# Performance work log

Measured on AMD Instinct MI355X. Metric: run time of the kernel, lower is better.

Reference implementation:

```python
import jax, jax.numpy as jnp
import numpy as np

H, KV, HD = 32, 4, 64
REP = H // KV
MAX_POS = 2048


def setup_inputs() -> dict:
    key = jax.random.key(0)
    ks = jax.random.split(key, 6)
    B, S, D = 2, 1024, 2048
    x = jax.random.normal(ks[0], (B, S, D), dtype=jnp.float32)
    wq = jax.random.normal(ks[1], (D, H * HD), dtype=jnp.float32) * 0.02
    wk = jax.random.normal(ks[2], (D, KV * HD), dtype=jnp.float32) * 0.02
    wv = jax.random.normal(ks[3], (D, KV * HD), dtype=jnp.float32) * 0.02
    wo = jax.random.normal(ks[4], (H * HD, D), dtype=jnp.float32) * 0.02
    # RoPE tables: [max_pos, head_dim//2]
    inv_freq = 1.0 / (10000.0 ** (np.arange(0, HD, 2, dtype=np.float32) / HD))
    angles = np.arange(MAX_POS, dtype=np.float32)[:, None] * inv_freq[None, :]
    cos = jnp.asarray(np.cos(angles), dtype=jnp.float32)
    sin = jnp.asarray(np.sin(angles), dtype=jnp.float32)
    # causal additive mask [S, S]
    row = jnp.arange(S)[:, None]
    col = jnp.arange(S)[None, :]
    mask = jnp.where(col <= row, 0.0, -1e9).astype(jnp.float32)
    return {"x": x, "wq": wq, "wk": wk, "wv": wv, "wo": wo,
            "cos": cos, "sin": sin, "mask": mask, "pos": 0}


def _rotate(t, c, s):
    # t: [B,S,Hx,HD]; c,s: [1,S,1,HD//2]
    half = t.shape[-1] // 2
    t1, t2 = t[..., :half], t[..., half:]
    return jnp.concatenate([t1 * c - t2 * s, t2 * c + t1 * s], axis=-1)


def reference(x, wq, wk, wv, wo, cos, sin, mask, pos):
    B, S, D = x.shape
    q = (x @ wq).reshape(B, S, H, HD)
    k = (x @ wk).reshape(B, S, KV, HD)
    v = (x @ wv).reshape(B, S, KV, HD)
    c = cos[pos:pos + S][None, :, None, :]
    s = sin[pos:pos + S][None, :, None, :]
    q = _rotate(q, c, s)
    k = _rotate(k, c, s)
    # prefill: cache[:, 0:S] == fresh k,v, kv_len == S
    # native GQA broadcast: group q heads by kv head instead of repeating k/v
    qg = q.reshape(B, S, KV, REP, HD)
    scores = jnp.einsum('bqkrd,bskd->bkrqs', qg, k) / jnp.sqrt(jnp.float32(HD))
    scores = scores + mask  # mask broadcasts over [B,KV,REP,S,S]
    attn = jax.nn.softmax(scores, axis=-1)
    out = jnp.einsum('bkrqs,bskd->bqkrd', attn, v).reshape(B, S, H * HD)
    return out @ wo
```

## Files before the change

### kernel.cpp

```cpp
#include <hip/hip_runtime.h>

#define B_ 2
#define S_ 1024
#define D_ 2048
#define H_ 32
#define KV_ 4
#define HD_ 64
#define NQKV 2560
#define KVB 64

typedef __attribute__((ext_vector_type(8))) short bf16x8;
typedef __attribute__((ext_vector_type(4))) float f32x4;
typedef __attribute__((ext_vector_type(16))) float f32x16;

__device__ __forceinline__ unsigned short f2bf(float f) {
  unsigned int u = __float_as_uint(f);
  u = (u + 0x7fffu + ((u >> 16) & 1u)) >> 16;
  return (unsigned short)u;
}

#define GLOAD_LDS(gp, lp) \
  __builtin_amdgcn_global_load_lds((const __attribute__((address_space(1))) void*)(gp), \
                                   (__attribute__((address_space(3))) void*)(lp), 16, 0, 0)

__global__ __launch_bounds__(256) void k_convert(const float* __restrict__ src,
                                                 unsigned short* __restrict__ dst, int n4) {
  int i = blockIdx.x * 256 + threadIdx.x;
  if (i >= n4) return;
  float4 v = ((const float4*)src)[i];
  ushort4 o;
  o.x = f2bf(v.x); o.y = f2bf(v.y); o.z = f2bf(v.z); o.w = f2bf(v.w);
  ((ushort4*)dst)[i] = o;
}

__global__ __launch_bounds__(256) void k_transpose4(const float* __restrict__ wq,
                                                    const float* __restrict__ wk,
                                                    const float* __restrict__ wv,
                                                    const float* __restrict__ wo,
                                                    unsigned short* __restrict__ wft,
                                                    unsigned short* __restrict__ wot) {
  __shared__ float tile[32][33];
  const int z = blockIdx.z;
  const float* src;
  unsigned short* dst;
  int N, roff;
  if (z == 0)      { src = wq; dst = wft; N = 2048; roff = 0; }
  else if (z == 1) { src = wk; dst = wft; N = 256;  roff = 2048; }
  else if (z == 2) { src = wv; dst = wft; N = 256;  roff = 2304; }
  else             { src = wo; dst = wot; N = 2048; roff = 0; }
  int n0 = blockIdx.x * 32, k0 = blockIdx.y * 32;
  if (n0 >= N) return;
  int tx = threadIdx.x & 31, ty = threadIdx.x >> 5;
  #pragma unroll
  for (int i = 0; i < 4; ++i)
    tile[ty + 8 * i][tx] = src[(size_t)(k0 + ty + 8 * i) * N + (n0 + tx)];
  __syncthreads();
  #pragma unroll
  for (int i = 0; i < 4; ++i)
    dst[(size_t)(roff + n0 + ty + 8 * i) * D_ + (k0 + tx)] = f2bf(tile[tx][ty + 8 * i]);
}

template <int BM, int BN, int MODE>
__global__ __launch_bounds__(256) void k_gemm(const unsigned short* __restrict__ A,
                                              const unsigned short* __restrict__ Bt,
                                              float* __restrict__ C,
                                              const float* __restrict__ cosT,
                                              const float* __restrict__ sinT,
                                              const int* __restrict__ posp,
                                              unsigned short* __restrict__ q_r,
                                              unsigned short* __restrict__ k_r,
                                              unsigned short* __restrict__ v_t,
                                              int M, int N, int K) {
  constexpr int MR = BM / 32;
  constexpr int NR = BN / 32;
  __shared__ alignas(16) unsigned short As[BM * 64];
  __shared__ alignas(16) unsigned short Bs[BN * 64];
  const int tid = threadIdx.x;
  const int wid = tid >> 6, lane = tid & 63;
  const int lo = lane & 15, hi = lane >> 4;
  const int m0 = blockIdx.y * BM, n0 = blockIdx.x * BN;
  const int wr = wid >> 1, wc = wid & 1;
  f32x4 acc[MR][NR] = {};

  const int nkt = K >> 6;
  for (int kt = 0; kt < nkt; ++kt) {
    __syncthreads();
    #pragma unroll
    for (int u = tid; u < BM * 8; u += 256) {
      int row = u >> 3, ch = u & 7, chs = ch ^ (row & 7);
      GLOAD_LDS(A + (size_t)(m0 + row) * K + kt * 64 + chs * 8, As + u * 8);
    }
    #pragma unroll
    for (int u = tid; u < BN * 8; u += 256) {
      int row = u >> 3, ch = u & 7, chs = ch ^ (row & 7);
      GLOAD_LDS(Bt + (size_t)(n0 + row) * K + kt * 64 + chs * 8, Bs + u * 8);
    }
    __syncthreads();
    #pragma unroll
    for (int ks = 0; ks < 2; ++ks) {
      const int chs = (ks * 4 + hi) ^ (lo & 7);
      bf16x8 a[MR], b[NR];
      #pragma unroll
      for (int m = 0; m < MR; ++m) {
        int row = wr * (BM / 2) + m * 16 + lo;
        a[m] = *(const bf16x8*)(As + row * 64 + chs * 8);
      }
      #pragma unroll
      for (int n = 0; n < NR; ++n) {
        int row = wc * (BN / 2) + n * 16 + lo;
        b[n] = *(const bf16x8*)(Bs + row * 64 + chs * 8);
      }
      #pragma unroll
      for (int m = 0; m < MR; ++m)
        #pragma unroll
        for (int n = 0; n < NR; ++n)
          acc[m][n] = __builtin_amdgcn_mfma_f32_16x16x32_bf16(a[m], b[n], acc[m][n], 0, 0, 0);
    }
  }

  if (MODE == 0) {
    const int cr = hi * 4;
    #pragma unroll
    for (int m = 0; m < MR; ++m)
      #pragma unroll
      for (int n = 0; n < NR; ++n) {
        int col = n0 + wc * (BN / 2) + n * 16 + lo;
        int rowb = m0 + wr * (BM / 2) + m * 16 + cr;
        #pragma unroll
        for (int r = 0; r < 4; ++r)
          C[(size_t)(rowb + r) * N + col] = acc[m][n][r];
      }
  } else {
    const int col0 = n0 + wc * (BN / 2);
    const int pos = posp[0];
    if (col0 < 2048) {
      const int h = col0 >> 6;
      #pragma unroll
      for (int m = 0; m < MR; ++m)
        #pragma unroll
        for (int r = 0; r < 4; ++r) {
          int row = m0 + wr * (BM / 2) + m * 16 + hi * 4 + r;
          int s = row & (S_ - 1), b = row >> 10;
          unsigned short* base = q_r + ((size_t)(b * H_ + h) * S_ + s) * HD_;
          #pragma unroll
          for (int np = 0; np < 2; ++np) {
            int i = np * 16 + lo;
            float t1 = acc[m][np][r], t2 = acc[m][np + 2][r];
            float c = cosT[(size_t)(pos + s) * 32 + i];
            float sn = sinT[(size_t)(pos + s) * 32 + i];
            base[i] = f2bf((t1 * c - t2 * sn) * 0.125f);
            base[i + 32] = f2bf((t2 * c + t1 * sn) * 0.125f);
          }
        }
    } else if (col0 < 2304) {
      const int g = (col0 - 2048) >> 6;
      #pragma unroll
      for (int m = 0; m < MR; ++m)
        #pragma unroll
        for (int r = 0; r < 4; ++r) {
          int row = m0 + wr * (BM / 2) + m * 16 + hi * 4 + r;
          int s = row & (S_ - 1), b = row >> 10;
          unsigned short* base = k_r + ((size_t)(b * KV_ + g) * S_ + s) * HD_;
          #pragma unroll
          for (int np = 0; np < 2; ++np) {
            int i = np * 16 + lo;
            float t1 = acc[m][np][r], t2 = acc[m][np + 2][r];
            float c = cosT[(size_t)(pos + s) * 32 + i];
            float sn = sinT[(size_t)(pos + s) * 32 + i];
            base[i] = f2bf(t1 * c - t2 * sn);
            base[i + 32] = f2bf(t2 * c + t1 * sn);
          }
        }
    } else {
      const int g = (col0 - 2304) >> 6;
      #pragma unroll
      for (int m = 0; m < MR; ++m) {
        int row0 = m0 + wr * (BM / 2) + m * 16 + hi * 4;
        int s0 = row0 & (S_ - 1), b = row0 >> 10;
        #pragma unroll
        for (int n = 0; n < NR; ++n) {
          int d = n * 16 + lo;
          ushort4 o;
          o.x = f2bf(acc[m][n][0]);
          o.y = f2bf(acc[m][n][1]);
          o.z = f2bf(acc[m][n][2]);
          o.w = f2bf(acc[m][n][3]);
          *(ushort4*)(v_t + ((size_t)(b * KV_ + g) * HD_ + d) * S_ + s0) = o;
        }
      }
    }
  }
}

__global__ __launch_bounds__(256) void k_attn(const unsigned short* __restrict__ qr,
                                              const unsigned short* __restrict__ kr,
                                              const unsigned short* __restrict__ vt,
                                              unsigned short* __restrict__ ao) {
  __shared__ alignas(16) unsigned short k_lds[2][KVB * HD_];
  __shared__ alignas(16) unsigned short v_lds[2][HD_ * KVB];
  const int tid = threadIdx.x;
  const int wid = tid >> 6, lane = tid & 63;
  const int l31 = lane & 31, hi5 = lane >> 5;

  const int fid = blockIdx.x + 8 * blockIdx.y + 256 * blockIdx.z;
  const int half = fid >> 8, u0 = fid & 255;
  const int i4 = u0 >> 6, hb = u0 & 63;
  const int qt = half ? 7 - i4 : i4;
  const int h = hb >> 1, b = hb & 1, g = h >> 3;

  const int q_abs = qt * 128 + wid * 32 + l31;
  const int nch = 2 * qt + 2;

  const unsigned short* qrow = qr + ((size_t)(b * H_ + h) * S_ + q_abs) * HD_;
  bf16x8 qf[4];
  #pragma unroll
  for (int ks = 0; ks < 4; ++ks)
    qf[ks] = *(const bf16x8*)(qrow + ks * 16 + hi5 * 8);

  const unsigned short* kbase = kr + (size_t)(b * KV_ + g) * S_ * HD_;
  const unsigned short* vbase = vt + (size_t)(b * KV_ + g) * HD_ * S_;

  f32x16 oacc[2] = {};
  float mrun = -1e30f, ls = 0.f;
  int buf = 0;

  auto stage = [&](int c, int bi) {
    const int j0 = c * KVB;
    #pragma unroll
    for (int ii = 0; ii < 2; ++ii) {
      int uu = ii * 256 + tid;
      int r = uu >> 3, ch = uu & 7, chs = ch ^ (r & 7);
      GLOAD_LDS(kbase + (size_t)(j0 + r) * HD_ + chs * 8, k_lds[bi] + uu * 8);
    }
    #pragma unroll
    for (int ii = 0; ii < 2; ++ii) {
      int uu = ii * 256 + tid;
      int d = uu >> 3, ch = uu & 7, chs = ch ^ (d & 7);
      GLOAD_LDS(vbase + (size_t)d * S_ + j0 + chs * 8, v_lds[bi] + uu * 8);
    }
  };

  stage(0, 0);
  __syncthreads();

  for (int c = 0; c < nch; ++c) {
    if (c + 1 < nch) stage(c + 1, buf ^ 1);
    const unsigned short* kl = k_lds[buf];
    const unsigned short* vl = v_lds[buf];
    const int j0 = c * KVB;

    f32x16 st[2] = {};
    __builtin_amdgcn_s_setprio(1);
    #pragma unroll
    for (int ks = 0; ks < 4; ++ks) {
      const int chs = ((ks * 2 + hi5) ^ (l31 & 7)) * 8;
      #pragma unroll
      for (int jt = 0; jt < 2; ++jt) {
        bf16x8 kf = *(const bf16x8*)(kl + (jt * 32 + l31) * HD_ + chs);
        st[jt] = __builtin_amdgcn_mfma_f32_32x32x16_bf16(kf, qf[ks], st[jt], 0, 0, 0);
      }
    }
    __builtin_amdgcn_s_setprio(0);

    float pmax = -1e30f;
    if (c >= nch - 2) {
      #pragma unroll
      for (int jt = 0; jt < 2; ++jt)
        #pragma unroll
        for (int r = 0; r < 16; ++r) {
          int j_abs = j0 + jt * 32 + (r & 3) + 8 * (r >> 2) + 4 * hi5;
          if (j_abs > q_abs) st[jt][r] = -1e30f;
          pmax = fmaxf(pmax, st[jt][r]);
        }
    } else {
      #pragma unroll
      for (int jt = 0; jt < 2; ++jt)
        #pragma unroll
        for (int r = 0; r < 16; ++r) pmax = fmaxf(pmax, st[jt][r]);
    }
    pmax = fmaxf(pmax, __shfl_xor(pmax, 32, 64));
    float mn = fmaxf(mrun, pmax);
    float scale = __expf(mrun - mn);
    float lsl = 0.f;
    #pragma unroll
    for (int jt = 0; jt < 2; ++jt)
      #pragma unroll
      for (int r = 0; r < 16; ++r) {
        float e = __expf(st[jt][r] - mn);
        st[jt][r] = e;
        lsl += e;
      }
    ls = ls * scale + lsl;
    mrun = mn;
    #pragma unroll
    for (int dt = 0; dt < 2; ++dt)
      #pragma unroll
      for (int r = 0; r < 16; ++r) oacc[dt][r] *= scale;

    unsigned int pk[2][4][2];
    #pragma unroll
    for (int jt = 0; jt < 2; ++jt)
      #pragma unroll
      for (int qd = 0; qd < 4; ++qd) {
        pk[jt][qd][0] = (unsigned int)f2bf(st[jt][qd * 4 + 0]) |
                        ((unsigned int)f2bf(st[jt][qd * 4 + 1]) << 16);
        pk[jt][qd][1] = (unsigned int)f2bf(st[jt][qd * 4 + 2]) |
                        ((unsigned int)f2bf(st[jt][qd * 4 + 3]) << 16);
      }

    bf16x8 pf[4];
    #pragma unroll
    for (int jt = 0; jt < 2; ++jt) {
      unsigned int ex0a = hi5 ? pk[jt][0][0] : pk[jt][1][0];
      unsigned int ex0b = hi5 ? pk[jt][0][1] : pk[jt][1][1];
      unsigned int ex1a = hi5 ? pk[jt][2][0] : pk[jt][3][0];
      unsigned int ex1b = hi5 ? pk[jt][2][1] : pk[jt][3][1];
      unsigned int rA0 = (unsigned int)__shfl_xor((int)ex0a, 32, 64);
      unsigned int rA1 = (unsigned int)__shfl_xor((int)ex0b, 32, 64);
      unsigned int rB0 = (unsigned int)__shfl_xor((int)ex1a, 32, 64);
      unsigned int rB1 = (unsigned int)__shfl_xor((int)ex1b, 32, 64);
      union { unsigned int w[4]; bf16x8 v; } fe, fo;
      if (hi5) {
        fe.w[0] = rA0; fe.w[1] = rA1; fe.w[2] = pk[jt][1][0]; fe.w[3] = pk[jt][1][1];
        fo.w[0] = rB0; fo.w[1] = rB1; fo.w[2] = pk[jt][3][0]; fo.w[3] = pk[jt][3][1];
      } else {
        fe.w[0] = pk[jt][0][0]; fe.w[1] = pk[jt][0][1]; fe.w[2] = rA0; fe.w[3] = rA1;
        fo.w[0] = pk[jt][2][0]; fo.w[1] = pk[jt][2][1]; fo.w[2] = rB0; fo.w[3] = rB1;
      }
      pf[jt * 2 + 0] = fe.v;
      pf[jt * 2 + 1] = fo.v;
    }

    __builtin_amdgcn_s_setprio(1);
    #pragma unroll
    for (int ks = 0; ks < 4; ++ks) {
      const int chs = ((ks * 2 + hi5) ^ (l31 & 7)) * 8;
      #pragma unroll
      for (int dt = 0; dt < 2; ++dt) {
        bf16x8 vf = *(const bf16x8*)(vl + (dt * 32 + l31) * KVB + chs);
        oacc[dt] = __builtin_amdgcn_mfma_f32_32x32x16_bf16(vf, pf[ks], oacc[dt], 0, 0, 0);
      }
    }
    __builtin_amdgcn_s_setprio(0);

    __syncthreads();
    buf ^= 1;
  }

  float tot = ls + __shfl_xor(ls, 32, 64);
  float inv = 1.f / tot;
  unsigned short* orow = ao + (size_t)(b * S_ + q_abs) * (H_ * HD_) + h * HD_;
  #pragma unroll
  for (int dt = 0; dt < 2; ++dt)
    #pragma unroll
    for (int rg = 0; rg < 4; ++rg) {
      ushort4 o;
      o.x = f2bf(oacc[dt][rg * 4 + 0] * inv);
      o.y = f2bf(oacc[dt][rg * 4 + 1] * inv);
      o.z = f2bf(oacc[dt][rg * 4 + 2] * inv);
      o.w = f2bf(oacc[dt][rg * 4 + 3] * inv);
      *(ushort4*)(orow + dt * 32 + rg * 8 + hi5 * 4) = o;
    }
}

extern "C" void kernel_launch(void* const* d_in, const int* in_sizes, int n_in,
                              void* d_out, int out_size, void* d_ws, size_t ws_size,
                              hipStream_t stream) {
  const float* x    = (const float*)d_in[0];
  const float* wq   = (const float*)d_in[1];
  const float* wk   = (const float*)d_in[2];
  const float* wv   = (const float*)d_in[3];
  const float* wo   = (const float*)d_in[4];
  const float* cosT = (const float*)d_in[5];
  const float* sinT = (const float*)d_in[6];
  const int*   posp = (const int*)d_in[8];
  float* out = (float*)d_out;

  char* ws = (char*)d_ws;
  size_t off = 0;
  auto alloc = [&](size_t bytes) {
    char* p = ws + off;
    off += (bytes + 255) & ~(size_t)255;
    return p;
  };
  unsigned short* xb  = (unsigned short*)alloc((size_t)B_ * S_ * D_ * 2);
  unsigned short* wft = (unsigned short*)alloc((size_t)NQKV * D_ * 2);
  unsigned short* wot = (unsigned short*)alloc((size_t)D_ * D_ * 2);
  unsigned short* q_r = (unsigned short*)alloc((size_t)B_ * H_ * S_ * HD_ * 2);
  unsigned short* k_r = (unsigned short*)alloc((size_t)B_ * KV_ * S_ * HD_ * 2);
  unsigned short* v_t = (unsigned short*)alloc((size_t)B_ * KV_ * HD_ * S_ * 2);
  unsigned short* ao  = (unsigned short*)alloc((size_t)B_ * S_ * H_ * HD_ * 2);
  if (off > ws_size) return;

  k_convert<<<(B_ * S_ * D_ / 4 + 255) / 256, 256, 0, stream>>>(x, xb, B_ * S_ * D_ / 4);
  k_transpose4<<<dim3(D_ / 32, D_ / 32, 4), 256, 0, stream>>>(wq, wk, wv, wo, wft, wot);

  k_gemm<64, 128, 1><<<dim3(NQKV / 128, (B_ * S_) / 64), 256, 0, stream>>>(
      xb, wft, nullptr, cosT, sinT, posp, q_r, k_r, v_t, B_ * S_, NQKV, D_);

  k_attn<<<dim3(8, 32, 2), 256, 0, stream>>>(q_r, k_r, v_t, ao);

  k_gemm<64, 128, 0><<<dim3(D_ / 128, (B_ * S_) / 64), 256, 0, stream>>>(
      ao, wot, out, nullptr, nullptr, nullptr, nullptr, nullptr, nullptr, B_ * S_, D_, D_);
}
```

Measured before the change: 114.6 us.

## Shrink attention blocks to 64 queries, fold log2e into Q, use exp2 and packed bf16 converts

The attention kernel now runs 128-thread blocks that each cover 64 query rows, launched on a 64x16 grid with the longest causal tiles scheduled first. This replaces the 256-thread, 128-row blocks and their remapped tile order, aiming for finer load balance and more resident blocks. The Q projection epilogue folds log2(e) into the 1/sqrt(d) scale so softmax can use the hardware exp2, and the rescale of the output accumulator is skipped whenever no lane's running max grows. Global and LDS addresses are precomputed once, and bf16 packing uses v_cvt_pk_bf16_f32 instead of manual rounding. Each block now reloads K/V tiles for half as many queries, which doubles total K/V staging traffic.

```diff
diff --git a/kernel.cpp b/kernel.cpp
--- a/kernel.cpp
+++ b/kernel.cpp
@@ -17,6 +17,14 @@
   unsigned int u = __float_as_uint(f);
   u = (u + 0x7fffu + ((u >> 16) & 1u)) >> 16;
   return (unsigned short)u;
+}
+__device__ __forceinline__ unsigned int cvt_pk_bf16(float a, float b) {
+  unsigned int r;
+  asm("v_cvt_pk_bf16_f32 %0, %1, %2" : "=v"(r) : "v"(a), "v"(b));
+  return r;
+}
+__device__ __forceinline__ float exp2f_fast(float x) {
+  return __builtin_amdgcn_exp2f(x);
 }
 
 #define GLOAD_LDS(gp, lp) \
@@ -133,6 +141,7 @@
   } else {
     const int col0 = n0 + wc * (BN / 2);
     const int pos = posp[0];
+    const float qsc = 0.125f * 1.44269504f;
     if (col0 < 2048) {
       const int h = col0 >> 6;
       #pragma unroll
@@ -148,8 +157,8 @@
             float t1 = acc[m][np][r], t2 = acc[m][np + 2][r];
             float c = cosT[(size_t)(pos + s) * 32 + i];
             float sn = sinT[(size_t)(pos + s) * 32 + i];
-            base[i] = f2bf((t1 * c - t2 * sn) * 0.125f);
-            base[i + 32] = f2bf((t2 * c + t1 * sn) * 0.125f);
+            base[i] = f2bf((t1 * c - t2 * sn) * qsc);
+            base[i + 32] = f2bf((t2 * c + t1 * sn) * qsc);
           }
         }
     } else if (col0 < 2304) {
@@ -192,24 +201,20 @@
   }
 }
 
-__global__ __launch_bounds__(256) void k_attn(const unsigned short* __restrict__ qr,
+__global__ __launch_bounds__(128) void k_attn(const unsigned short* __restrict__ qr,
                                               const unsigned short* __restrict__ kr,
                                               const unsigned short* __restrict__ vt,
                                               unsigned short* __restrict__ ao) {
-  __shared__ alignas(16) unsigned short k_lds[2][KVB * HD_];
-  __shared__ alignas(16) unsigned short v_lds[2][HD_ * KVB];
+  __shared__ alignas(16) unsigned short k_lds[2 * KVB * HD_];
+  __shared__ alignas(16) unsigned short v_lds[2 * HD_ * KVB];
   const int tid = threadIdx.x;
   const int wid = tid >> 6, lane = tid & 63;
   const int l31 = lane & 31, hi5 = lane >> 5;
-
-  const int fid = blockIdx.x + 8 * blockIdx.y + 256 * blockIdx.z;
-  const int half = fid >> 8, u0 = fid & 255;
-  const int i4 = u0 >> 6, hb = u0 & 63;
-  const int qt = half ? 7 - i4 : i4;
-  const int h = hb >> 1, b = hb & 1, g = h >> 3;
-
-  const int q_abs = qt * 128 + wid * 32 + l31;
-  const int nch = 2 * qt + 2;
+  const int bh = blockIdx.x;
+  const int h = bh >> 1, b = bh & 1, g = h >> 3;
+  const int qt = 15 - (int)blockIdx.y;
+  const int nch = qt + 1;
+  const int q_abs = qt * 64 + wid * 32 + l31;
 
   const unsigned short* qrow = qr + ((size_t)(b * H_ + h) * S_ + q_abs) * HD_;
   bf16x8 qf[4];
@@ -219,25 +224,34 @@
 
   const unsigned short* kbase = kr + (size_t)(b * KV_ + g) * S_ * HD_;
   const unsigned short* vbase = vt + (size_t)(b * KV_ + g) * HD_ * S_;
+
+  const unsigned short* kg[4];
+  const unsigned short* vg[4];
+  int ldo[4];
+  #pragma unroll
+  for (int ii = 0; ii < 4; ++ii) {
+    int uu = ii * 128 + tid;
+    int r = uu >> 3, ch = uu & 7, chs = ch ^ (r & 7);
+    kg[ii] = kbase + r * HD_ + chs * 8;
+    vg[ii] = vbase + (size_t)r * S_ + chs * 8;
+    ldo[ii] = uu * 8;
+  }
+  int chs8[4];
+  #pragma unroll
+  for (int ks = 0; ks < 4; ++ks) chs8[ks] = ((ks * 2 + hi5) ^ (l31 & 7)) * 8;
+  const int krow = l31 * 64;
 
   f32x16 oacc[2] = {};
   float mrun = -1e30f, ls = 0.f;
   int buf = 0;
 
   auto stage = [&](int c, int bi) {
-    const int j0 = c * KVB;
-    #pragma unroll
-    for (int ii = 0; ii < 2; ++ii) {
-      int uu = ii * 256 + tid;
-      int r = uu >> 3, ch = uu & 7, chs = ch ^ (r & 7);
-      GLOAD_LDS(kbase + (size_t)(j0 + r) * HD_ + chs * 8, k_lds[bi] + uu * 8);
-    }
-    #pragma unroll
-    for (int ii = 0; ii < 2; ++ii) {
-      int uu = ii * 256 + tid;
-      int d = uu >> 3, ch = uu & 7, chs = ch ^ (d & 7);
-      GLOAD_LDS(vbase + (size_t)d * S_ + j0 + chs * 8, v_lds[bi] + uu * 8);
-    }
+    #pragma unroll
+    for (int ii = 0; ii < 4; ++ii)
+      GLOAD_LDS(kg[ii] + (size_t)c * (KVB * HD_), k_lds + bi * 4096 + ldo[ii]);
+    #pragma unroll
+    for (int ii = 0; ii < 4; ++ii)
+      GLOAD_LDS(vg[ii] + (size_t)c * KVB, v_lds + bi * 4096 + ldo[ii]);
   };
 
   stage(0, 0);
@@ -245,25 +259,23 @@
 
   for (int c = 0; c < nch; ++c) {
     if (c + 1 < nch) stage(c + 1, buf ^ 1);
-    const unsigned short* kl = k_lds[buf];
-    const unsigned short* vl = v_lds[buf];
+    const unsigned short* kl = k_lds + buf * 4096;
+    const unsigned short* vl = v_lds + buf * 4096;
     const int j0 = c * KVB;
 
     f32x16 st[2] = {};
     __builtin_amdgcn_s_setprio(1);
     #pragma unroll
-    for (int ks = 0; ks < 4; ++ks) {
-      const int chs = ((ks * 2 + hi5) ^ (l31 & 7)) * 8;
+    for (int ks = 0; ks < 4; ++ks)
       #pragma unroll
       for (int jt = 0; jt < 2; ++jt) {
-        bf16x8 kf = *(const bf16x8*)(kl + (jt * 32 + l31) * HD_ + chs);
+        bf16x8 kf = *(const bf16x8*)(kl + jt * 2048 + krow + chs8[ks]);
         st[jt] = __builtin_amdgcn_mfma_f32_32x32x16_bf16(kf, qf[ks], st[jt], 0, 0, 0);
       }
-    }
     __builtin_amdgcn_s_setprio(0);
 
     float pmax = -1e30f;
-    if (c >= nch - 2) {
+    if (c == nch - 1) {
       #pragma unroll
       for (int jt = 0; jt < 2; ++jt)
         #pragma unroll
@@ -279,33 +291,36 @@
         for (int r = 0; r < 16; ++r) pmax = fmaxf(pmax, st[jt][r]);
     }
     pmax = fmaxf(pmax, __shfl_xor(pmax, 32, 64));
-    float mn = fmaxf(mrun, pmax);
-    float scale = __expf(mrun - mn);
-    float lsl = 0.f;
+
+    if (__any(pmax > mrun)) {
+      float mn = fmaxf(mrun, pmax);
+      float scale = exp2f_fast(mrun - mn);
+      ls *= scale;
+      #pragma unroll
+      for (int dt = 0; dt < 2; ++dt)
+        #pragma unroll
+        for (int r = 0; r < 16; ++r) oacc[dt][r] *= scale;
+      mrun = mn;
+    }
+    float ls0 = 0.f, ls1 = 0.f, ls2 = 0.f, ls3 = 0.f;
     #pragma unroll
     for (int jt = 0; jt < 2; ++jt)
       #pragma unroll
       for (int r = 0; r < 16; ++r) {
-        float e = __expf(st[jt][r] - mn);
+        float e = exp2f_fast(st[jt][r] - mrun);
         st[jt][r] = e;
-        lsl += e;
-      }
-    ls = ls * scale + lsl;
-    mrun = mn;
-    #pragma unroll
-    for (int dt = 0; dt < 2; ++dt)
-      #pragma unroll
-      for (int r = 0; r < 16; ++r) oacc[dt][r] *= scale;
+        if ((r & 3) == 0) ls0 += e; else if ((r & 3) == 1) ls1 += e;
+        else if ((r & 3) == 2) ls2 += e; else ls3 += e;
+      }
+    ls += (ls0 + ls1) + (ls2 + ls3);
 
     unsigned int pk[2][4][2];
     #pragma unroll
     for (int jt = 0; jt < 2; ++jt)
       #pragma unroll
       for (int qd = 0; qd < 4; ++qd) {
-        pk[jt][qd][0] = (unsigned int)f2bf(st[jt][qd * 4 + 0]) |
-                        ((unsigned int)f2bf(st[jt][qd * 4 + 1]) << 16);
-        pk[jt][qd][1] = (unsigned int)f2bf(st[jt][qd * 4 + 2]) |
-                        ((unsigned int)f2bf(st[jt][qd * 4 + 3]) << 16);
+        pk[jt][qd][0] = cvt_pk_bf16(st[jt][qd * 4 + 0], st[jt][qd * 4 + 1]);
+        pk[jt][qd][1] = cvt_pk_bf16(st[jt][qd * 4 + 2], st[jt][qd * 4 + 3]);
       }
 
     bf16x8 pf[4];
@@ -333,14 +348,12 @@
 
     __builtin_amdgcn_s_setprio(1);
     #pragma unroll
-    for (int ks = 0; ks < 4; ++ks) {
-      const int chs = ((ks * 2 + hi5) ^ (l31 & 7)) * 8;
+    for (int ks = 0; ks < 4; ++ks)
       #pragma unroll
       for (int dt = 0; dt < 2; ++dt) {
-        bf16x8 vf = *(const bf16x8*)(vl + (dt * 32 + l31) * KVB + chs);
+        bf16x8 vf = *(const bf16x8*)(vl + dt * 2048 + krow + chs8[ks]);
         oacc[dt] = __builtin_amdgcn_mfma_f32_32x32x16_bf16(vf, pf[ks], oacc[dt], 0, 0, 0);
       }
-    }
     __builtin_amdgcn_s_setprio(0);
 
     __syncthreads();
@@ -354,12 +367,10 @@
   for (int dt = 0; dt < 2; ++dt)
     #pragma unroll
     for (int rg = 0; rg < 4; ++rg) {
-      ushort4 o;
-      o.x = f2bf(oacc[dt][rg * 4 + 0] * inv);
-      o.y = f2bf(oacc[dt][rg * 4 + 1] * inv);
-      o.z = f2bf(oacc[dt][rg * 4 + 2] * inv);
-      o.w = f2bf(oacc[dt][rg * 4 + 3] * inv);
-      *(ushort4*)(orow + dt * 32 + rg * 8 + hi5 * 4) = o;
+      uint2 w;
+      w.x = cvt_pk_bf16(oacc[dt][rg * 4 + 0] * inv, oacc[dt][rg * 4 + 1] * inv);
+      w.y = cvt_pk_bf16(oacc[dt][rg * 4 + 2] * inv, oacc[dt][rg * 4 + 3] * inv);
+      *(uint2*)(orow + dt * 32 + rg * 8 + hi5 * 4) = w;
     }
 }
 
@@ -398,7 +409,7 @@
   k_gemm<64, 128, 1><<<dim3(NQKV / 128, (B_ * S_) / 64), 256, 0, stream>>>(
       xb, wft, nullptr, cosT, sinT, posp, q_r, k_r, v_t, B_ * S_, NQKV, D_);
 
-  k_attn<<<dim3(8, 32, 2), 256, 0, stream>>>(q_r, k_r, v_t, ao);
+  k_attn<<<dim3(64, 16), 128, 0, stream>>>(q_r, k_r, v_t, ao);
 
   k_gemm<64, 128, 0><<<dim3(D_ / 128, (B_ * S_) / 64), 256, 0, stream>>>(
       ao, wot, out, nullptr, nullptr, nullptr, nullptr, nullptr, nullptr, B_ * S_, D_, D_);
```

After: 110.4 us. 3.6% less time.
